# Kernel tuning notes

Measured on AMD Instinct MI355X. Metric: run time of the kernel, lower is better.

## Reference

```python
import jax, jax.numpy as jnp
import numpy as np
import math

P, DD, N, E, NDRUGS = 256, 128, 1024, 250000, 200000
BASELINE = 6.0

def _prelu(x, a):
    return jnp.where(x >= 0, x, a * x)

def _lrelu(x):
    return jnp.where(x >= 0, x, 0.2 * x)

def _lin(x, W, b):
    return x @ W.T + b

def setup_inputs() -> dict:
    key = jax.random.key(0)
    ks = jax.random.split(key, 40)
    f32 = jnp.float32
    inp = {}
    inp["target_features"] = jax.random.normal(ks[0], (P,), f32)
    inp["form_features"] = jax.random.normal(ks[1], (N, P), f32)
    inp["role_features"] = jax.random.normal(ks[2], (N, P), f32)
    inp["form_neighbors"] = jnp.arange(N, dtype=jnp.int32)
    inp["form_binds_src"] = jax.random.randint(ks[3], (E,), 0, N, jnp.int32)
    inp["form_binds_dst"] = jax.random.randint(ks[4], (E,), 0, NDRUGS, jnp.int32)
    inp["form_binds_y"] = jax.random.uniform(ks[5], (E,), f32, 4.0, 9.0)
    inp["role_neighbors"] = jnp.arange(N, dtype=jnp.int32)
    inp["role_binds_src"] = jax.random.randint(ks[6], (E,), 0, N, jnp.int32)
    inp["role_binds_dst"] = jax.random.randint(ks[7], (E,), 0, NDRUGS, jnp.int32)
    inp["role_binds_y"] = jax.random.uniform(ks[8], (E,), f32, 4.0, 9.0)
    inp["drug_features"] = jax.random.normal(ks[9], (NDRUGS, DD), f32)
    s = 0.02
    # prot_refiner: Linear(P,P) -> PReLU -> Linear(P,P)
    inp["Wr1"] = jax.random.normal(ks[10], (P, P), f32) * s
    inp["br1"] = jnp.zeros((P,), f32)
    inp["ar1"] = jnp.asarray(0.25, f32)
    inp["Wr2"] = jax.random.normal(ks[11], (P, P), f32) * s
    inp["br2"] = jnp.zeros((P,), f32)
    # q/k/v projections
    inp["Wq"] = jax.random.normal(ks[12], (DD, P), f32) * s
    inp["bq"] = jnp.zeros((DD,), f32)
    inp["Wk"] = jax.random.normal(ks[13], (DD, DD), f32) * s
    inp["bk"] = jnp.zeros((DD,), f32)
    inp["Wv"] = jax.random.normal(ks[14], (DD, DD), f32) * s
    inp["bv"] = jnp.zeros((DD,), f32)
    inp["layer_emb"] = jax.random.normal(ks[15], (2, 16), f32) * s
    # attn_net: (2P+16)->128->64->1 with LeakyReLU(0.2)
    inp["Wa1"] = jax.random.normal(ks[16], (128, 2 * P + 16), f32) * s
    inp["ba1"] = jnp.zeros((128,), f32)
    inp["Wa2"] = jax.random.normal(ks[17], (64, 128), f32) * s
    inp["ba2"] = jnp.zeros((64,), f32)
    inp["Wa3"] = jax.random.normal(ks[18], (1, 64), f32) * s
    inp["ba3"] = jnp.zeros((1,), f32)
    # integration_mlp: Linear(DD,P) -> PReLU -> Linear(P,P)
    inp["Wi1"] = jax.random.normal(ks[19], (P, DD), f32) * s
    inp["bi1"] = jnp.zeros((P,), f32)
    inp["ai"] = jnp.asarray(0.25, f32)
    inp["Wi2"] = jax.random.normal(ks[20], (P, P), f32) * s
    inp["bi2"] = jnp.zeros((P,), f32)
    inp["ln_g"] = jnp.ones((P,), f32)
    inp["ln_b"] = jnp.zeros((P,), f32)
    return inp

def reference(target_features, form_features, role_features, form_neighbors,
              form_binds_src, form_binds_dst, form_binds_y,
              role_neighbors, role_binds_src, role_binds_dst, role_binds_y,
              drug_features,
              Wr1, br1, ar1, Wr2, br2, Wq, bq, Wk, bk, Wv, bv, layer_emb,
              Wa1, ba1, Wa2, ba2, Wa3, ba3, Wi1, bi1, ai, Wi2, bi2, ln_g, ln_b):
    def refine(x):
        return _lin(_prelu(_lin(x, Wr1, br1), ar1), Wr2, br2)

    zt = refine(target_features)          # [P]
    zf = refine(form_features)            # [N, P]
    zr = refine(role_features)            # [N, P]
    Qv = _lin(zt, Wq, bq)                 # [DD]

    def build_msgs(neighbors, src, dst, y):
        # segment id for each edge: position of src in (sorted) neighbor_ids;
        # edges whose src is not a neighbor go to the dummy segment n.
        n = neighbors.shape[0]
        pos = jnp.clip(jnp.searchsorted(neighbors, src), 0, n - 1)
        seg = jnp.where(neighbors[pos] == src, pos, n)
        d = drug_features[dst]                                # [E, DD] gather
        K = _lin(d, Wk, bk)                                   # [E, DD]
        V = _lin(d, Wv, bv) * (y - BASELINE)[:, None]         # [E, DD]
        s = (K @ Qv) / math.sqrt(DD)                          # [E]
        nseg = n + 1
        m = jax.ops.segment_max(s, seg, num_segments=nseg)    # per-neighbor max
        ex = jnp.exp(s - m[seg])                              # stable softmax numerator
        den = jax.ops.segment_sum(ex, seg, num_segments=nseg)[:n]          # [N]
        num = jax.ops.segment_sum(ex[:, None] * V, seg, num_segments=nseg)[:n]  # [N, DD]
        return jnp.where(den[:, None] > 0, num / jnp.maximum(den, 1e-30)[:, None], 0.0)

    form_msgs = build_msgs(form_neighbors, form_binds_src, form_binds_dst, form_binds_y)
    role_msgs = build_msgs(role_neighbors, role_binds_src, role_binds_dst, role_binds_y)

    def attn(zn, layer_id):
        n = zn.shape[0]
        le = jnp.broadcast_to(layer_emb[layer_id], (n, 16))
        zt_e = jnp.broadcast_to(zt, (n, P))
        x = jnp.concatenate([zt_e, zn, le], axis=-1)          # [N, 2P+16]
        h = _lrelu(_lin(x, Wa1, ba1))
        h = _lrelu(_lin(h, Wa2, ba2))
        return _lin(h, Wa3, ba3)                              # [N, 1]

    all_msgs = jnp.concatenate([form_msgs, role_msgs], axis=0)   # [2N, DD]
    all_attn = jnp.concatenate([attn(zf, 0), attn(zr, 1)], axis=0)  # [2N, 1]
    w = jax.nn.softmax(all_attn, axis=0)
    v_prior = jnp.sum(w * all_msgs, axis=0)                   # [DD]
    integ = _lin(_prelu(_lin(v_prior, Wi1, bi1), ai), Wi2, bi2)
    x = zt + integ
    mu = jnp.mean(x, axis=-1, keepdims=True)
    var = jnp.var(x, axis=-1, keepdims=True)
    z = (x - mu) / jnp.sqrt(var + 1e-5) * ln_g + ln_b
    return (z, form_msgs, role_msgs)
```

## Files before the change

kernel.cpp:

```cpp
#include <hip/hip_runtime.h>

#define NP 256
#define NDD 128
#define NN 1024
#define NE 250000
#define SB 62

__global__ __launch_bounds__(256) void refine_kernel(
    const float* __restrict__ tgt, const float* __restrict__ formf, const float* __restrict__ rolef,
    const float* __restrict__ Wr1, const float* __restrict__ br1, const float* __restrict__ ar1,
    const float* __restrict__ Wr2, const float* __restrict__ br2,
    float* __restrict__ zt, float* __restrict__ zf, float* __restrict__ zr)
{
  __shared__ float X[4][NP];
  __shared__ float H[4][NP];
  const int t = threadIdx.x;
  const int base = blockIdx.x * 4;
  #pragma unroll
  for (int r = 0; r < 4; r++){
    int row = base + r;
    if (row < 2*NN + 1){
      const float* xp;
      if (row == 0)        xp = tgt;
      else if (row <= NN)  xp = formf + (size_t)(row-1)*NP;
      else                 xp = rolef + (size_t)(row-NN-1)*NP;
      X[r][t] = xp[t];
    } else {
      X[r][t] = 0.f;
    }
  }
  __syncthreads();
  const float a1 = ar1[0];
  float acc[4];
  #pragma unroll
  for (int r = 0; r < 4; r++) acc[r] = 0.f;
  const float4* w1p = reinterpret_cast<const float4*>(Wr1) + t*(NP/4);
  for (int k4 = 0; k4 < NP/4; k4++){
    float4 w = w1p[k4];
    #pragma unroll
    for (int r = 0; r < 4; r++){
      float4 xv = *reinterpret_cast<const float4*>(&X[r][k4*4]);
      acc[r] = fmaf(w.x, xv.x, acc[r]);
      acc[r] = fmaf(w.y, xv.y, acc[r]);
      acc[r] = fmaf(w.z, xv.z, acc[r]);
      acc[r] = fmaf(w.w, xv.w, acc[r]);
    }
  }
  const float b1 = br1[t];
  #pragma unroll
  for (int r = 0; r < 4; r++){
    float h = acc[r] + b1;
    H[r][t] = h >= 0.f ? h : a1*h;
  }
  __syncthreads();
  #pragma unroll
  for (int r = 0; r < 4; r++) acc[r] = 0.f;
  const float4* w2p = reinterpret_cast<const float4*>(Wr2) + t*(NP/4);
  for (int k4 = 0; k4 < NP/4; k4++){
    float4 w = w2p[k4];
    #pragma unroll
    for (int r = 0; r < 4; r++){
      float4 hv = *reinterpret_cast<const float4*>(&H[r][k4*4]);
      acc[r] = fmaf(w.x, hv.x, acc[r]);
      acc[r] = fmaf(w.y, hv.y, acc[r]);
      acc[r] = fmaf(w.z, hv.z, acc[r]);
      acc[r] = fmaf(w.w, hv.w, acc[r]);
    }
  }
  const float b2 = br2[t];
  #pragma unroll
  for (int r = 0; r < 4; r++){
    int row = base + r;
    if (row < 2*NN + 1){
      float v = acc[r] + b2;
      float* op;
      if (row == 0)        op = zt;
      else if (row <= NN)  op = zf + (size_t)(row-1)*NP;
      else                 op = zr + (size_t)(row-NN-1)*NP;
      op[t] = v;
    }
  }
}

__global__ __launch_bounds__(128) void qk_kernel(
    const float* __restrict__ zt,
    const float* __restrict__ Wq, const float* __restrict__ bq,
    const float* __restrict__ Wk, const float* __restrict__ bk,
    float* __restrict__ qk, float* __restrict__ s0)
{
  __shared__ float Z[NP];
  __shared__ float Q[NDD];
  __shared__ float red[NDD];
  int t = threadIdx.x;
  Z[t] = zt[t]; Z[t+128] = zt[t+128];
  __syncthreads();
  float acc = 0.f;
  const float4* wq = reinterpret_cast<const float4*>(Wq) + t*(NP/4);
  for (int k4 = 0; k4 < NP/4; k4++){
    float4 w = wq[k4];
    float4 zv = *reinterpret_cast<const float4*>(&Z[k4*4]);
    acc = fmaf(w.x, zv.x, fmaf(w.y, zv.y, fmaf(w.z, zv.z, fmaf(w.w, zv.w, acc))));
  }
  float qv = acc + bq[t];
  Q[t] = qv;
  __syncthreads();
  float a2 = 0.f;
  for (int j = 0; j < NDD; j++) a2 = fmaf(Wk[j*NDD + t], Q[j], a2);
  const float rs = 0.08838834764831845f;
  qk[t] = a2 * rs;
  red[t] = bk[t] * qv;
  __syncthreads();
  for (int o = 64; o; o >>= 1){ if (t < o) red[t] += red[t+o]; __syncthreads(); }
  if (t == 0) s0[0] = red[0] * rs;
}

__device__ __forceinline__ int seg_of(const int* NB, int s){
  if ((unsigned)s < NN && NB[s] == s) return s;
  int lo = 0, hi = NN;
  while (lo < hi){ int mid = (lo+hi)>>1; if (NB[mid] < s) lo = mid+1; else hi = mid; }
  return lo < NN ? lo : NN-1;
}

__global__ __launch_bounds__(1024) void hist_kernel(
    const int* __restrict__ neighF, const int* __restrict__ srcF,
    const int* __restrict__ neighR, const int* __restrict__ srcR,
    int* __restrict__ count)
{
  __shared__ int NB[NN];
  __shared__ int lh[NN];
  int bi = blockIdx.x;
  int role = bi >= SB ? 1 : 0;
  int blk = bi - role*SB;
  const int* neigh = role ? neighR : neighF;
  const int* src   = role ? srcR   : srcF;
  int* cnt = count + role*NN;
  int t = threadIdx.x;
  NB[t] = neigh[t];
  lh[t] = 0;
  __syncthreads();
  #pragma unroll
  for (int i = 0; i < 4; i++){
    int e = blk*4096 + i*1024 + t;
    if (e < NE){
      int s = src[e];
      int pos = seg_of(NB, s);
      if (NB[pos] == s) atomicAdd(&lh[pos], 1);
    }
  }
  __syncthreads();
  int c = lh[t];
  if (c > 0) atomicAdd(&cnt[t], c);
}

__global__ __launch_bounds__(1024) void scan_kernel(
    const int* __restrict__ count, int* __restrict__ offsets, int* __restrict__ cursor)
{
  __shared__ int s[NN];
  int l = blockIdx.x;
  int t = threadIdx.x;
  int c = count[l*NN + t];
  s[t] = c; __syncthreads();
  for (int o = 1; o < NN; o <<= 1){
    int v = (t >= o) ? s[t-o] : 0;
    __syncthreads();
    s[t] += v;
    __syncthreads();
  }
  int ex = s[t] - c;
  offsets[l*NN + t] = ex;
  cursor[l*NN + t]  = ex;
}

__global__ __launch_bounds__(1024) void scatter_kernel(
    const int* __restrict__ neighF, const int* __restrict__ srcF,
    const int* __restrict__ dstF, const float* __restrict__ yF,
    const int* __restrict__ neighR, const int* __restrict__ srcR,
    const int* __restrict__ dstR, const float* __restrict__ yR,
    int* __restrict__ cursor, int2* __restrict__ edges)
{
  __shared__ int NB[NN];
  __shared__ int lcur[NN];
  __shared__ int lbase[NN];
  int bi = blockIdx.x;
  int role = bi >= SB ? 1 : 0;
  int blk = bi - role*SB;
  const int* neigh = role ? neighR : neighF;
  const int* src   = role ? srcR   : srcF;
  const int* dst   = role ? dstR   : dstF;
  const float* yb  = role ? yR     : yF;
  int* cur  = cursor + role*NN;
  int2* ed  = edges  + (size_t)role*NE;
  int t = threadIdx.x;
  NB[t] = neigh[t];
  lcur[t] = 0;
  __syncthreads();
  int segr[4], locr[4]; int2 edr[4];
  #pragma unroll
  for (int i = 0; i < 4; i++){
    int e = blk*4096 + i*1024 + t;
    segr[i] = -1;
    if (e < NE){
      int s = src[e];
      int pos = seg_of(NB, s);
      if (NB[pos] == s){
        segr[i] = pos;
        edr[i]  = make_int2(dst[e], __float_as_int(yb[e]));
        locr[i] = atomicAdd(&lcur[pos], 1);
      }
    }
  }
  __syncthreads();
  int c = lcur[t];
  if (c > 0) lbase[t] = atomicAdd(&cur[t], c);
  __syncthreads();
  #pragma unroll
  for (int i = 0; i < 4; i++){
    if (segr[i] >= 0){
      ed[(size_t)(lbase[segr[i]] + locr[i])] = edr[i];
    }
  }
}

__global__ __launch_bounds__(256) void seg_kernel(
    const float* __restrict__ drug,
    const int2* __restrict__ edges,
    const int* __restrict__ offsets, const int* __restrict__ count,
    const float* __restrict__ qk, const float* __restrict__ s0p,
    float* __restrict__ g, float* __restrict__ den, float* __restrict__ cfac)
{
  int b = blockIdx.x;
  int tid = threadIdx.x;
  int w = tid >> 6, lane = tid & 63, l32 = lane & 31, half = lane >> 5;
  int off = offsets[b], cnt = count[b];
  int l = b >> 10;
  const int2* eb = edges + (size_t)l*NE;
  float4 q = reinterpret_cast<const float4*>(qk)[l32];
  float s0 = s0p[0];
  int chunk = (cnt + 3) >> 2;
  int start = w*chunk;
  int end = min(start + chunk, cnt);
  float dn = 0.f, cc = 0.f;
  float4 ga = make_float4(0.f,0.f,0.f,0.f);
  for (int i = start; i < end; i += 8){
    int dstp[4]; float yp[4]; bool vp[4];
    #pragma unroll
    for (int p2 = 0; p2 < 4; p2++){
      int idx = i + 2*p2 + half;
      bool v = idx < end;
      int2 e = eb[off + (v ? idx : start)];
      dstp[p2] = e.x; yp[p2] = __int_as_float(e.y); vp[p2] = v;
    }
    float4 dv[4];
    #pragma unroll
    for (int p2 = 0; p2 < 4; p2++){
      dv[p2] = reinterpret_cast<const float4*>(drug + (size_t)dstp[p2]*NDD)[l32];
    }
    #pragma unroll
    for (int p2 = 0; p2 < 4; p2++){
      float4 d = dv[p2];
      float s = fmaf(d.x, q.x, fmaf(d.y, q.y, fmaf(d.z, q.z, d.w*q.w)));
      s += __shfl_xor(s, 16, 64);
      s += __shfl_xor(s,  8, 64);
      s += __shfl_xor(s,  4, 64);
      s += __shfl_xor(s,  2, 64);
      s += __shfl_xor(s,  1, 64);
      float ex = vp[p2] ? __expf(s + s0) : 0.f;
      float wv = ex * (yp[p2] - 6.0f);
      dn += ex; cc += wv;
      ga.x = fmaf(wv, d.x, ga.x);
      ga.y = fmaf(wv, d.y, ga.y);
      ga.z = fmaf(wv, d.z, ga.z);
      ga.w = fmaf(wv, d.w, ga.w);
    }
  }
  __shared__ float4 sG[8][32];
  __shared__ float sD[8], sC[8];
  int slot = w*2 + half;
  sG[slot][l32] = ga;
  if (l32 == 0){ sD[slot] = dn; sC[slot] = cc; }
  __syncthreads();
  if (tid < NDD){
    int a = tid >> 2, c = tid & 3;
    float v = 0.f;
    #pragma unroll
    for (int k = 0; k < 8; k++)
      v += reinterpret_cast<const float*>(&sG[k][a])[c];
    g[(size_t)b*NDD + tid] = v;
    if (tid == 0){
      float ds = 0.f, cs = 0.f;
      #pragma unroll
      for (int k = 0; k < 8; k++){ ds += sD[k]; cs += sC[k]; }
      den[b] = ds; cfac[b] = cs;
    }
  }
}

__global__ __launch_bounds__(128) void msgs_kernel(
    const float* __restrict__ g, const float* __restrict__ den, const float* __restrict__ cfac,
    const float* __restrict__ Wv, const float* __restrict__ bv,
    float* __restrict__ msgsf, float* __restrict__ outm)
{
  __shared__ float G[8][NDD];
  int t = threadIdx.x;
  int base = blockIdx.x*8;
  #pragma unroll
  for (int r = 0; r < 8; r++) G[r][t] = g[(size_t)(base+r)*NDD + t];
  __syncthreads();
  float acc[8];
  #pragma unroll
  for (int r = 0; r < 8; r++) acc[r] = 0.f;
  const float4* wv4 = reinterpret_cast<const float4*>(Wv) + t*(NDD/4);
  for (int k4 = 0; k4 < NDD/4; k4++){
    float4 w = wv4[k4];
    #pragma unroll
    for (int r = 0; r < 8; r++){
      float4 gv = *reinterpret_cast<const float4*>(&G[r][k4*4]);
      acc[r] = fmaf(w.x, gv.x, acc[r]);
      acc[r] = fmaf(w.y, gv.y, acc[r]);
      acc[r] = fmaf(w.z, gv.z, acc[r]);
      acc[r] = fmaf(w.w, gv.w, acc[r]);
    }
  }
  float bvj = bv[t];
  #pragma unroll
  for (int r = 0; r < 8; r++){
    int row = base + r;
    float dn = den[row];
    float v = 0.f;
    if (dn > 0.f) v = (acc[r] + bvj*cfac[row]) / fmaxf(dn, 1e-30f);
    msgsf[(size_t)row*NDD + t] = v;
    outm [(size_t)row*NDD + t] = v;
  }
}

__global__ __launch_bounds__(256) void attn_kernel(
    const float* __restrict__ zt, const float* __restrict__ zf, const float* __restrict__ zr,
    const float* __restrict__ lemb,
    const float* __restrict__ Wa1, const float* __restrict__ ba1,
    const float* __restrict__ Wa2, const float* __restrict__ ba2,
    const float* __restrict__ Wa3, const float* __restrict__ ba3,
    float* __restrict__ attn)
{
  __shared__ float X[8][528];
  __shared__ float H1[8][NDD];
  int t = threadIdx.x;
  int tt = t & 127, grp = t >> 7;
  int base = blockIdx.x*8;
  for (int r = 0; r < 8; r++){
    int i = base + r;
    int layer = i >> 10, nn = i & (NN-1);
    const float* zn = (layer == 0) ? (zf + (size_t)nn*NP) : (zr + (size_t)nn*NP);
    for (int idx = t; idx < 528; idx += 256){
      float v;
      if (idx < NP)        v = zt[idx];
      else if (idx < 2*NP) v = zn[idx - NP];
      else                 v = lemb[layer*16 + (idx - 2*NP)];
      X[r][idx] = v;
    }
  }
  __syncthreads();
  float acc[4];
  #pragma unroll
  for (int r = 0; r < 4; r++) acc[r] = 0.f;
  const float4* w1 = reinterpret_cast<const float4*>(Wa1) + tt*(528/4);
  for (int k4 = 0; k4 < 132; k4++){
    float4 w = w1[k4];
    #pragma unroll
    for (int r = 0; r < 4; r++){
      float4 xv = *reinterpret_cast<const float4*>(&X[grp*4 + r][k4*4]);
      acc[r] = fmaf(w.x, xv.x, acc[r]);
      acc[r] = fmaf(w.y, xv.y, acc[r]);
      acc[r] = fmaf(w.z, xv.z, acc[r]);
      acc[r] = fmaf(w.w, xv.w, acc[r]);
    }
  }
  float b1 = ba1[tt];
  #pragma unroll
  for (int r = 0; r < 4; r++){
    float h = acc[r] + b1;
    H1[grp*4 + r][tt] = h >= 0.f ? h : 0.2f*h;
  }
  __syncthreads();
  if (tt < 64){
    float acc2[4];
    #pragma unroll
    for (int r = 0; r < 4; r++) acc2[r] = 0.f;
    const float4* w2 = reinterpret_cast<const float4*>(Wa2) + tt*(NDD/4);
    for (int k4 = 0; k4 < NDD/4; k4++){
      float4 w = w2[k4];
      #pragma unroll
      for (int r = 0; r < 4; r++){
        float4 hv = *reinterpret_cast<const float4*>(&H1[grp*4 + r][k4*4]);
        acc2[r] = fmaf(w.x, hv.x, acc2[r]);
        acc2[r] = fmaf(w.y, hv.y, acc2[r]);
        acc2[r] = fmaf(w.z, hv.z, acc2[r]);
        acc2[r] = fmaf(w.w, hv.w, acc2[r]);
      }
    }
    float b2 = ba2[tt];
    float w3 = Wa3[tt];
    float b3 = ba3[0];
    #pragma unroll
    for (int r = 0; r < 4; r++){
      float h = acc2[r] + b2;
      h = h >= 0.f ? h : 0.2f*h;
      float p = w3 * h;
      #pragma unroll
      for (int o = 32; o; o >>= 1) p += __shfl_xor(p, o, 64);
      if (tt == 0) attn[base + grp*4 + r] = p + b3;
    }
  }
}

__global__ __launch_bounds__(1024) void vprior_kernel(
    const float* __restrict__ attn, const float* __restrict__ msgsf, float* __restrict__ vp)
{
  __shared__ float A[2*NN];
  __shared__ float red[1024];
  __shared__ float Pp[8][NDD];
  int t = threadIdx.x;
  A[t] = attn[t]; A[t+1024] = attn[t+1024];
  __syncthreads();
  float mx = fmaxf(A[t], A[t+1024]);
  red[t] = mx; __syncthreads();
  for (int o = 512; o; o >>= 1){ if (t < o) red[t] = fmaxf(red[t], red[t+o]); __syncthreads(); }
  float M = red[0]; __syncthreads();
  float sm = __expf(A[t] - M) + __expf(A[t+1024] - M);
  red[t] = sm; __syncthreads();
  for (int o = 512; o; o >>= 1){ if (t < o) red[t] += red[t+o]; __syncthreads(); }
  float inv = 1.f / red[0]; __syncthreads();
  A[t]      = __expf(A[t]      - M) * inv;
  A[t+1024] = __expf(A[t+1024] - M) * inv;
  __syncthreads();
  int j = t & 127, grp = t >> 7;
  float acc = 0.f;
  int i0 = grp * 256;
  for (int i = i0; i < i0 + 256; i++) acc = fmaf(A[i], msgsf[(size_t)i*NDD + j], acc);
  Pp[grp][j] = acc;
  __syncthreads();
  if (t < NDD){
    float v = 0.f;
    #pragma unroll
    for (int gg = 0; gg < 8; gg++) v += Pp[gg][t];
    vp[t] = v;
  }
}

__global__ __launch_bounds__(256) void final_kernel(
    const float* __restrict__ vprior, const float* __restrict__ zt,
    const float* __restrict__ Wi1, const float* __restrict__ bi1, const float* __restrict__ ai,
    const float* __restrict__ Wi2, const float* __restrict__ bi2,
    const float* __restrict__ ln_g, const float* __restrict__ ln_b,
    float* __restrict__ zout)
{
  __shared__ float V[NDD];
  __shared__ float T1[NP];
  __shared__ float red[NP];
  int t = threadIdx.x;
  if (t < NDD) V[t] = vprior[t];
  __syncthreads();
  float acc = 0.f;
  const float4* w1 = reinterpret_cast<const float4*>(Wi1) + t*(NDD/4);
  for (int k4 = 0; k4 < NDD/4; k4++){
    float4 w = w1[k4];
    float4 vv = *reinterpret_cast<const float4*>(&V[k4*4]);
    acc = fmaf(w.x, vv.x, fmaf(w.y, vv.y, fmaf(w.z, vv.z, fmaf(w.w, vv.w, acc))));
  }
  float h = acc + bi1[t];
  float a = ai[0];
  T1[t] = h >= 0.f ? h : a*h;
  __syncthreads();
  float acc2 = 0.f;
  const float4* w2 = reinterpret_cast<const float4*>(Wi2) + t*(NP/4);
  for (int k4 = 0; k4 < NP/4; k4++){
    float4 w = w2[k4];
    float4 hv = *reinterpret_cast<const float4*>(&T1[k4*4]);
    acc2 = fmaf(w.x, hv.x, fmaf(w.y, hv.y, fmaf(w.z, hv.z, fmaf(w.w, hv.w, acc2))));
  }
  float x = zt[t] + acc2 + bi2[t];
  red[t] = x; __syncthreads();
  for (int o = 128; o; o >>= 1){ if (t < o) red[t] += red[t+o]; __syncthreads(); }
  float mu = red[0] * (1.f/256.f); __syncthreads();
  float d = x - mu;
  red[t] = d*d; __syncthreads();
  for (int o = 128; o; o >>= 1){ if (t < o) red[t] += red[t+o]; __syncthreads(); }
  float var = red[0] * (1.f/256.f);
  float zz = d * rsqrtf(var + 1e-5f) * ln_g[t] + ln_b[t];
  zout[t] = zz;
}

extern "C" void kernel_launch(void* const* d_in, const int* in_sizes, int n_in,
                              void* d_out, int out_size, void* d_ws, size_t ws_size,
                              hipStream_t stream)
{
  const float* tgt    = (const float*)d_in[0];
  const float* formf  = (const float*)d_in[1];
  const float* rolef  = (const float*)d_in[2];
  const int* fneigh   = (const int*)d_in[3];
  const int* fsrc     = (const int*)d_in[4];
  const int* fdst     = (const int*)d_in[5];
  const float* fy     = (const float*)d_in[6];
  const int* rneigh   = (const int*)d_in[7];
  const int* rsrc     = (const int*)d_in[8];
  const int* rdst     = (const int*)d_in[9];
  const float* ry     = (const float*)d_in[10];
  const float* drug   = (const float*)d_in[11];
  const float* Wr1 = (const float*)d_in[12];
  const float* br1 = (const float*)d_in[13];
  const float* ar1 = (const float*)d_in[14];
  const float* Wr2 = (const float*)d_in[15];
  const float* br2 = (const float*)d_in[16];
  const float* Wq  = (const float*)d_in[17];
  const float* bq  = (const float*)d_in[18];
  const float* Wk  = (const float*)d_in[19];
  const float* bk  = (const float*)d_in[20];
  const float* Wv  = (const float*)d_in[21];
  const float* bv  = (const float*)d_in[22];
  const float* lemb= (const float*)d_in[23];
  const float* Wa1 = (const float*)d_in[24];
  const float* ba1 = (const float*)d_in[25];
  const float* Wa2 = (const float*)d_in[26];
  const float* ba2 = (const float*)d_in[27];
  const float* Wa3 = (const float*)d_in[28];
  const float* ba3 = (const float*)d_in[29];
  const float* Wi1 = (const float*)d_in[30];
  const float* bi1 = (const float*)d_in[31];
  const float* ai  = (const float*)d_in[32];
  const float* Wi2 = (const float*)d_in[33];
  const float* bi2 = (const float*)d_in[34];
  const float* lng = (const float*)d_in[35];
  const float* lnb = (const float*)d_in[36];
  (void)in_sizes; (void)n_in; (void)out_size; (void)ws_size;

  float* ws = (float*)d_ws;
  float* zt_     = ws + 0;
  float* zf_     = ws + 256;
  float* zr_     = ws + 262400;
  float* qk_     = ws + 524544;
  float* s0_     = ws + 524672;
  float* attn_   = ws + 524800;
  float* vprior_ = ws + 526848;
  float* den_    = ws + 527104;
  float* cfac_   = ws + 529152;
  float* g_      = ws + 531200;
  float* msgsf_  = ws + 793344;
  int*   count_  = (int*)(ws + 1055488);
  int*   offs_   = (int*)(ws + 1057536);
  int*   cursor_ = (int*)(ws + 1059584);
  int2*  edges_  = (int2*)(ws + 1061632);

  hipMemsetAsync(count_, 0, 2*NN*sizeof(int), stream);

  refine_kernel<<<513, 256, 0, stream>>>(tgt, formf, rolef, Wr1, br1, ar1, Wr2, br2,
                                         zt_, zf_, zr_);
  qk_kernel<<<1, 128, 0, stream>>>(zt_, Wq, bq, Wk, bk, qk_, s0_);

  hist_kernel<<<2*SB, 1024, 0, stream>>>(fneigh, fsrc, rneigh, rsrc, count_);
  scan_kernel<<<2, 1024, 0, stream>>>(count_, offs_, cursor_);
  scatter_kernel<<<2*SB, 1024, 0, stream>>>(fneigh, fsrc, fdst, fy,
                                            rneigh, rsrc, rdst, ry,
                                            cursor_, edges_);

  seg_kernel<<<2*NN, 256, 0, stream>>>(drug, edges_, offs_, count_, qk_, s0_,
                                       g_, den_, cfac_);

  msgs_kernel<<<2*NN/8, 128, 0, stream>>>(g_, den_, cfac_, Wv, bv,
                                          msgsf_, (float*)d_out + NP);
  attn_kernel<<<2*NN/8, 256, 0, stream>>>(zt_, zf_, zr_, lemb,
                                          Wa1, ba1, Wa2, ba2, Wa3, ba3, attn_);
  vprior_kernel<<<1, 1024, 0, stream>>>(attn_, msgsf_, vprior_);
  final_kernel<<<1, 256, 0, stream>>>(vprior_, zt_, Wi1, bi1, ai, Wi2, bi2,
                                      lng, lnb, (float*)d_out);
}
```

Measured before the change: 389.2 us.

## Fuse small kernels to cut launch count: refine+qk, scan into scatter, attn+msgs

Merges qk into refine block 0 and moves the count/cursor zeroing into refine blocks 1 and 2, which replaces the memset. The prefix scan now runs redundantly in every scatter block, with a zeroed cursor added to the computed offsets. attn and msgs become one launch that splits its blocks by role, and vprior is fused with final. Together these remove four launches and one memset, at the cost of the scan being repeated in every scatter block and a single-block serial tail.

```diff
diff --git a/kernel.cpp b/kernel.cpp
--- a/kernel.cpp
+++ b/kernel.cpp
@@ -6,16 +6,32 @@
 #define NE 250000
 #define SB 62
 
-__global__ __launch_bounds__(256) void refine_kernel(
+__global__ __launch_bounds__(256) void refine_qk_kernel(
     const float* __restrict__ tgt, const float* __restrict__ formf, const float* __restrict__ rolef,
     const float* __restrict__ Wr1, const float* __restrict__ br1, const float* __restrict__ ar1,
     const float* __restrict__ Wr2, const float* __restrict__ br2,
-    float* __restrict__ zt, float* __restrict__ zf, float* __restrict__ zr)
+    const float* __restrict__ Wq, const float* __restrict__ bq,
+    const float* __restrict__ Wk, const float* __restrict__ bk,
+    float* __restrict__ zt, float* __restrict__ zf, float* __restrict__ zr,
+    float* __restrict__ qk, float* __restrict__ s0,
+    int* __restrict__ count, int* __restrict__ cursor0)
 {
   __shared__ float X[4][NP];
   __shared__ float H[4][NP];
+  __shared__ float Zs[NP];
+  __shared__ float Q[NDD];
+  __shared__ float red[NDD];
   const int t = threadIdx.x;
   const int base = blockIdx.x * 4;
+
+  if (blockIdx.x == 1){
+    #pragma unroll
+    for (int i = 0; i < 8; i++) count[t + i*256] = 0;
+  } else if (blockIdx.x == 2){
+    #pragma unroll
+    for (int i = 0; i < 8; i++) cursor0[t + i*256] = 0;
+  }
+
   #pragma unroll
   for (int r = 0; r < 4; r++){
     int row = base + r;
@@ -74,44 +90,40 @@
     if (row < 2*NN + 1){
       float v = acc[r] + b2;
       float* op;
-      if (row == 0)        op = zt;
+      if (row == 0){ op = zt; Zs[t] = v; }
       else if (row <= NN)  op = zf + (size_t)(row-1)*NP;
       else                 op = zr + (size_t)(row-NN-1)*NP;
       op[t] = v;
     }
   }
-}
-
-__global__ __launch_bounds__(128) void qk_kernel(
-    const float* __restrict__ zt,
-    const float* __restrict__ Wq, const float* __restrict__ bq,
-    const float* __restrict__ Wk, const float* __restrict__ bk,
-    float* __restrict__ qk, float* __restrict__ s0)
-{
-  __shared__ float Z[NP];
-  __shared__ float Q[NDD];
-  __shared__ float red[NDD];
-  int t = threadIdx.x;
-  Z[t] = zt[t]; Z[t+128] = zt[t+128];
-  __syncthreads();
-  float acc = 0.f;
-  const float4* wq = reinterpret_cast<const float4*>(Wq) + t*(NP/4);
-  for (int k4 = 0; k4 < NP/4; k4++){
-    float4 w = wq[k4];
-    float4 zv = *reinterpret_cast<const float4*>(&Z[k4*4]);
-    acc = fmaf(w.x, zv.x, fmaf(w.y, zv.y, fmaf(w.z, zv.z, fmaf(w.w, zv.w, acc))));
-  }
-  float qv = acc + bq[t];
-  Q[t] = qv;
-  __syncthreads();
-  float a2 = 0.f;
-  for (int j = 0; j < NDD; j++) a2 = fmaf(Wk[j*NDD + t], Q[j], a2);
-  const float rs = 0.08838834764831845f;
-  qk[t] = a2 * rs;
-  red[t] = bk[t] * qv;
-  __syncthreads();
-  for (int o = 64; o; o >>= 1){ if (t < o) red[t] += red[t+o]; __syncthreads(); }
-  if (t == 0) s0[0] = red[0] * rs;
+
+  if (blockIdx.x == 0){
+    __syncthreads();
+    if (t < NDD){
+      float a = 0.f;
+      const float4* wq = reinterpret_cast<const float4*>(Wq) + t*(NP/4);
+      for (int k4 = 0; k4 < NP/4; k4++){
+        float4 w = wq[k4];
+        float4 zv = *reinterpret_cast<const float4*>(&Zs[k4*4]);
+        a = fmaf(w.x, zv.x, fmaf(w.y, zv.y, fmaf(w.z, zv.z, fmaf(w.w, zv.w, a))));
+      }
+      float qv = a + bq[t];
+      Q[t] = qv;
+      red[t] = bk[t] * qv;
+    }
+    __syncthreads();
+    const float rs = 0.08838834764831845f;
+    if (t < NDD){
+      float a2 = 0.f;
+      for (int j = 0; j < NDD; j++) a2 = fmaf(Wk[j*NDD + t], Q[j], a2);
+      qk[t] = a2 * rs;
+    }
+    for (int o = 64; o; o >>= 1){
+      if (t < o) red[t] += red[t+o];
+      __syncthreads();
+    }
+    if (t == 0) s0[0] = red[0] * rs;
+  }
 }
 
 __device__ __forceinline__ int seg_of(const int* NB, int s){
@@ -152,34 +164,18 @@
   if (c > 0) atomicAdd(&cnt[t], c);
 }
 
-__global__ __launch_bounds__(1024) void scan_kernel(
-    const int* __restrict__ count, int* __restrict__ offsets, int* __restrict__ cursor)
-{
-  __shared__ int s[NN];
-  int l = blockIdx.x;
-  int t = threadIdx.x;
-  int c = count[l*NN + t];
-  s[t] = c; __syncthreads();
-  for (int o = 1; o < NN; o <<= 1){
-    int v = (t >= o) ? s[t-o] : 0;
-    __syncthreads();
-    s[t] += v;
-    __syncthreads();
-  }
-  int ex = s[t] - c;
-  offsets[l*NN + t] = ex;
-  cursor[l*NN + t]  = ex;
-}
-
 __global__ __launch_bounds__(1024) void scatter_kernel(
     const int* __restrict__ neighF, const int* __restrict__ srcF,
     const int* __restrict__ dstF, const float* __restrict__ yF,
     const int* __restrict__ neighR, const int* __restrict__ srcR,
     const int* __restrict__ dstR, const float* __restrict__ yR,
-    int* __restrict__ cursor, int2* __restrict__ edges)
+    const int* __restrict__ count, int* __restrict__ cursor0,
+    int* __restrict__ offsets, int2* __restrict__ edges)
 {
   __shared__ int NB[NN];
   __shared__ int lcur[NN];
+  __shared__ int sscan[NN];
+  __shared__ int obase[NN];
   __shared__ int lbase[NN];
   int bi = blockIdx.x;
   int role = bi >= SB ? 1 : 0;
@@ -188,12 +184,24 @@
   const int* src   = role ? srcR   : srcF;
   const int* dst   = role ? dstR   : dstF;
   const float* yb  = role ? yR     : yF;
-  int* cur  = cursor + role*NN;
-  int2* ed  = edges  + (size_t)role*NE;
+  int* cur0 = cursor0 + role*NN;
+  int2* ed  = edges   + (size_t)role*NE;
   int t = threadIdx.x;
   NB[t] = neigh[t];
   lcur[t] = 0;
-  __syncthreads();
+  int c0 = count[role*NN + t];
+  sscan[t] = c0;
+  __syncthreads();
+  for (int o = 1; o < NN; o <<= 1){
+    int v = (t >= o) ? sscan[t-o] : 0;
+    __syncthreads();
+    sscan[t] += v;
+    __syncthreads();
+  }
+  obase[t] = sscan[t] - c0;
+  if (blk == 0) offsets[role*NN + t] = sscan[t] - c0;
+  __syncthreads();
+
   int segr[4], locr[4]; int2 edr[4];
   #pragma unroll
   for (int i = 0; i < 4; i++){
@@ -211,7 +219,7 @@
   }
   __syncthreads();
   int c = lcur[t];
-  if (c > 0) lbase[t] = atomicAdd(&cur[t], c);
+  if (c > 0) lbase[t] = obase[t] + atomicAdd(&cur0[t], c);
   __syncthreads();
   #pragma unroll
   for (int i = 0; i < 4; i++){
@@ -295,129 +303,134 @@
   }
 }
 
-__global__ __launch_bounds__(128) void msgs_kernel(
-    const float* __restrict__ g, const float* __restrict__ den, const float* __restrict__ cfac,
-    const float* __restrict__ Wv, const float* __restrict__ bv,
-    float* __restrict__ msgsf, float* __restrict__ outm)
-{
-  __shared__ float G[8][NDD];
-  int t = threadIdx.x;
-  int base = blockIdx.x*8;
-  #pragma unroll
-  for (int r = 0; r < 8; r++) G[r][t] = g[(size_t)(base+r)*NDD + t];
-  __syncthreads();
-  float acc[8];
-  #pragma unroll
-  for (int r = 0; r < 8; r++) acc[r] = 0.f;
-  const float4* wv4 = reinterpret_cast<const float4*>(Wv) + t*(NDD/4);
-  for (int k4 = 0; k4 < NDD/4; k4++){
-    float4 w = wv4[k4];
-    #pragma unroll
-    for (int r = 0; r < 8; r++){
-      float4 gv = *reinterpret_cast<const float4*>(&G[r][k4*4]);
-      acc[r] = fmaf(w.x, gv.x, acc[r]);
-      acc[r] = fmaf(w.y, gv.y, acc[r]);
-      acc[r] = fmaf(w.z, gv.z, acc[r]);
-      acc[r] = fmaf(w.w, gv.w, acc[r]);
-    }
-  }
-  float bvj = bv[t];
-  #pragma unroll
-  for (int r = 0; r < 8; r++){
-    int row = base + r;
-    float dn = den[row];
-    float v = 0.f;
-    if (dn > 0.f) v = (acc[r] + bvj*cfac[row]) / fmaxf(dn, 1e-30f);
-    msgsf[(size_t)row*NDD + t] = v;
-    outm [(size_t)row*NDD + t] = v;
-  }
-}
-
-__global__ __launch_bounds__(256) void attn_kernel(
+__global__ __launch_bounds__(256) void attn_msgs_kernel(
     const float* __restrict__ zt, const float* __restrict__ zf, const float* __restrict__ zr,
     const float* __restrict__ lemb,
     const float* __restrict__ Wa1, const float* __restrict__ ba1,
     const float* __restrict__ Wa2, const float* __restrict__ ba2,
     const float* __restrict__ Wa3, const float* __restrict__ ba3,
-    float* __restrict__ attn)
-{
-  __shared__ float X[8][528];
-  __shared__ float H1[8][NDD];
+    const float* __restrict__ g, const float* __restrict__ den, const float* __restrict__ cfac,
+    const float* __restrict__ Wv, const float* __restrict__ bv,
+    float* __restrict__ attn, float* __restrict__ msgsf, float* __restrict__ outm)
+{
   int t = threadIdx.x;
   int tt = t & 127, grp = t >> 7;
-  int base = blockIdx.x*8;
-  for (int r = 0; r < 8; r++){
-    int i = base + r;
-    int layer = i >> 10, nn = i & (NN-1);
-    const float* zn = (layer == 0) ? (zf + (size_t)nn*NP) : (zr + (size_t)nn*NP);
-    for (int idx = t; idx < 528; idx += 256){
-      float v;
-      if (idx < NP)        v = zt[idx];
-      else if (idx < 2*NP) v = zn[idx - NP];
-      else                 v = lemb[layer*16 + (idx - 2*NP)];
-      X[r][idx] = v;
-    }
-  }
-  __syncthreads();
-  float acc[4];
-  #pragma unroll
-  for (int r = 0; r < 4; r++) acc[r] = 0.f;
-  const float4* w1 = reinterpret_cast<const float4*>(Wa1) + tt*(528/4);
-  for (int k4 = 0; k4 < 132; k4++){
-    float4 w = w1[k4];
-    #pragma unroll
-    for (int r = 0; r < 4; r++){
-      float4 xv = *reinterpret_cast<const float4*>(&X[grp*4 + r][k4*4]);
-      acc[r] = fmaf(w.x, xv.x, acc[r]);
-      acc[r] = fmaf(w.y, xv.y, acc[r]);
-      acc[r] = fmaf(w.z, xv.z, acc[r]);
-      acc[r] = fmaf(w.w, xv.w, acc[r]);
-    }
-  }
-  float b1 = ba1[tt];
-  #pragma unroll
-  for (int r = 0; r < 4; r++){
-    float h = acc[r] + b1;
-    H1[grp*4 + r][tt] = h >= 0.f ? h : 0.2f*h;
-  }
-  __syncthreads();
-  if (tt < 64){
-    float acc2[4];
-    #pragma unroll
-    for (int r = 0; r < 4; r++) acc2[r] = 0.f;
-    const float4* w2 = reinterpret_cast<const float4*>(Wa2) + tt*(NDD/4);
-    for (int k4 = 0; k4 < NDD/4; k4++){
-      float4 w = w2[k4];
+  if (blockIdx.x < 256){
+    __shared__ float X[8][528];
+    __shared__ float H1[8][NDD];
+    int base = blockIdx.x*8;
+    for (int r = 0; r < 8; r++){
+      int i = base + r;
+      int layer = i >> 10, nn = i & (NN-1);
+      const float* zn = (layer == 0) ? (zf + (size_t)nn*NP) : (zr + (size_t)nn*NP);
+      for (int idx = t; idx < 528; idx += 256){
+        float v;
+        if (idx < NP)        v = zt[idx];
+        else if (idx < 2*NP) v = zn[idx - NP];
+        else                 v = lemb[layer*16 + (idx - 2*NP)];
+        X[r][idx] = v;
+      }
+    }
+    __syncthreads();
+    float acc[4];
+    #pragma unroll
+    for (int r = 0; r < 4; r++) acc[r] = 0.f;
+    const float4* w1 = reinterpret_cast<const float4*>(Wa1) + tt*(528/4);
+    for (int k4 = 0; k4 < 132; k4++){
+      float4 w = w1[k4];
       #pragma unroll
       for (int r = 0; r < 4; r++){
-        float4 hv = *reinterpret_cast<const float4*>(&H1[grp*4 + r][k4*4]);
-        acc2[r] = fmaf(w.x, hv.x, acc2[r]);
-        acc2[r] = fmaf(w.y, hv.y, acc2[r]);
-        acc2[r] = fmaf(w.z, hv.z, acc2[r]);
-        acc2[r] = fmaf(w.w, hv.w, acc2[r]);
-      }
-    }
-    float b2 = ba2[tt];
-    float w3 = Wa3[tt];
-    float b3 = ba3[0];
+        float4 xv = *reinterpret_cast<const float4*>(&X[grp*4 + r][k4*4]);
+        acc[r] = fmaf(w.x, xv.x, acc[r]);
+        acc[r] = fmaf(w.y, xv.y, acc[r]);
+        acc[r] = fmaf(w.z, xv.z, acc[r]);
+        acc[r] = fmaf(w.w, xv.w, acc[r]);
+      }
+    }
+    float b1 = ba1[tt];
     #pragma unroll
     for (int r = 0; r < 4; r++){
-      float h = acc2[r] + b2;
-      h = h >= 0.f ? h : 0.2f*h;
-      float p = w3 * h;
+      float h = acc[r] + b1;
+      H1[grp*4 + r][tt] = h >= 0.f ? h : 0.2f*h;
+    }
+    __syncthreads();
+    if (tt < 64){
+      float acc2[4];
       #pragma unroll
-      for (int o = 32; o; o >>= 1) p += __shfl_xor(p, o, 64);
-      if (tt == 0) attn[base + grp*4 + r] = p + b3;
-    }
-  }
-}
-
-__global__ __launch_bounds__(1024) void vprior_kernel(
-    const float* __restrict__ attn, const float* __restrict__ msgsf, float* __restrict__ vp)
+      for (int r = 0; r < 4; r++) acc2[r] = 0.f;
+      const float4* w2 = reinterpret_cast<const float4*>(Wa2) + tt*(NDD/4);
+      for (int k4 = 0; k4 < NDD/4; k4++){
+        float4 w = w2[k4];
+        #pragma unroll
+        for (int r = 0; r < 4; r++){
+          float4 hv = *reinterpret_cast<const float4*>(&H1[grp*4 + r][k4*4]);
+          acc2[r] = fmaf(w.x, hv.x, acc2[r]);
+          acc2[r] = fmaf(w.y, hv.y, acc2[r]);
+          acc2[r] = fmaf(w.z, hv.z, acc2[r]);
+          acc2[r] = fmaf(w.w, hv.w, acc2[r]);
+        }
+      }
+      float b2 = ba2[tt];
+      float w3 = Wa3[tt];
+      float b3 = ba3[0];
+      #pragma unroll
+      for (int r = 0; r < 4; r++){
+        float h = acc2[r] + b2;
+        h = h >= 0.f ? h : 0.2f*h;
+        float p = w3 * h;
+        #pragma unroll
+        for (int o = 32; o; o >>= 1) p += __shfl_xor(p, o, 64);
+        if (tt == 0) attn[base + grp*4 + r] = p + b3;
+      }
+    }
+  } else {
+    __shared__ float G[8][NDD];
+    int base = (blockIdx.x - 256)*8;
+    #pragma unroll
+    for (int r = 0; r < 4; r++) G[grp*4 + r][tt] = g[(size_t)(base + grp*4 + r)*NDD + tt];
+    __syncthreads();
+    float acc[4];
+    #pragma unroll
+    for (int r = 0; r < 4; r++) acc[r] = 0.f;
+    const float4* wv4 = reinterpret_cast<const float4*>(Wv) + tt*(NDD/4);
+    for (int k4 = 0; k4 < NDD/4; k4++){
+      float4 w = wv4[k4];
+      #pragma unroll
+      for (int r = 0; r < 4; r++){
+        float4 gv = *reinterpret_cast<const float4*>(&G[grp*4 + r][k4*4]);
+        acc[r] = fmaf(w.x, gv.x, acc[r]);
+        acc[r] = fmaf(w.y, gv.y, acc[r]);
+        acc[r] = fmaf(w.z, gv.z, acc[r]);
+        acc[r] = fmaf(w.w, gv.w, acc[r]);
+      }
+    }
+    float bvj = bv[tt];
+    #pragma unroll
+    for (int r = 0; r < 4; r++){
+      int row = base + grp*4 + r;
+      float dn = den[row];
+      float v = 0.f;
+      if (dn > 0.f) v = (acc[r] + bvj*cfac[row]) / fmaxf(dn, 1e-30f);
+      msgsf[(size_t)row*NDD + tt] = v;
+      outm [(size_t)row*NDD + tt] = v;
+    }
+  }
+}
+
+__global__ __launch_bounds__(1024) void vprior_final_kernel(
+    const float* __restrict__ attn, const float* __restrict__ msgsf,
+    const float* __restrict__ zt,
+    const float* __restrict__ Wi1, const float* __restrict__ bi1, const float* __restrict__ ai,
+    const float* __restrict__ Wi2, const float* __restrict__ bi2,
+    const float* __restrict__ ln_g, const float* __restrict__ ln_b,
+    float* __restrict__ zout)
 {
   __shared__ float A[2*NN];
   __shared__ float red[1024];
   __shared__ float Pp[8][NDD];
+  __shared__ float V[NDD];
+  __shared__ float T1[NP];
+  __shared__ float red2[NP];
   int t = threadIdx.x;
   A[t] = attn[t]; A[t+1024] = attn[t+1024];
   __syncthreads();
@@ -442,51 +455,46 @@
     float v = 0.f;
     #pragma unroll
     for (int gg = 0; gg < 8; gg++) v += Pp[gg][t];
-    vp[t] = v;
-  }
-}
-
-__global__ __launch_bounds__(256) void final_kernel(
-    const float* __restrict__ vprior, const float* __restrict__ zt,
-    const float* __restrict__ Wi1, const float* __restrict__ bi1, const float* __restrict__ ai,
-    const float* __restrict__ Wi2, const float* __restrict__ bi2,
-    const float* __restrict__ ln_g, const float* __restrict__ ln_b,
-    float* __restrict__ zout)
-{
-  __shared__ float V[NDD];
-  __shared__ float T1[NP];
-  __shared__ float red[NP];
-  int t = threadIdx.x;
-  if (t < NDD) V[t] = vprior[t];
-  __syncthreads();
-  float acc = 0.f;
-  const float4* w1 = reinterpret_cast<const float4*>(Wi1) + t*(NDD/4);
-  for (int k4 = 0; k4 < NDD/4; k4++){
-    float4 w = w1[k4];
-    float4 vv = *reinterpret_cast<const float4*>(&V[k4*4]);
-    acc = fmaf(w.x, vv.x, fmaf(w.y, vv.y, fmaf(w.z, vv.z, fmaf(w.w, vv.w, acc))));
-  }
-  float h = acc + bi1[t];
-  float a = ai[0];
-  T1[t] = h >= 0.f ? h : a*h;
-  __syncthreads();
-  float acc2 = 0.f;
-  const float4* w2 = reinterpret_cast<const float4*>(Wi2) + t*(NP/4);
-  for (int k4 = 0; k4 < NP/4; k4++){
-    float4 w = w2[k4];
-    float4 hv = *reinterpret_cast<const float4*>(&T1[k4*4]);
-    acc2 = fmaf(w.x, hv.x, fmaf(w.y, hv.y, fmaf(w.z, hv.z, fmaf(w.w, hv.w, acc2))));
-  }
-  float x = zt[t] + acc2 + bi2[t];
-  red[t] = x; __syncthreads();
-  for (int o = 128; o; o >>= 1){ if (t < o) red[t] += red[t+o]; __syncthreads(); }
-  float mu = red[0] * (1.f/256.f); __syncthreads();
+    V[t] = v;
+  }
+  __syncthreads();
+  float x = 0.f;
+  if (t < NP){
+    float a1 = 0.f;
+    const float4* w1 = reinterpret_cast<const float4*>(Wi1) + t*(NDD/4);
+    for (int k4 = 0; k4 < NDD/4; k4++){
+      float4 w = w1[k4];
+      float4 vv = *reinterpret_cast<const float4*>(&V[k4*4]);
+      a1 = fmaf(w.x, vv.x, fmaf(w.y, vv.y, fmaf(w.z, vv.z, fmaf(w.w, vv.w, a1))));
+    }
+    float h = a1 + bi1[t];
+    float a = ai[0];
+    T1[t] = h >= 0.f ? h : a*h;
+  }
+  __syncthreads();
+  if (t < NP){
+    float a2 = 0.f;
+    const float4* w2 = reinterpret_cast<const float4*>(Wi2) + t*(NP/4);
+    for (int k4 = 0; k4 < NP/4; k4++){
+      float4 w = w2[k4];
+      float4 hv = *reinterpret_cast<const float4*>(&T1[k4*4]);
+      a2 = fmaf(w.x, hv.x, fmaf(w.y, hv.y, fmaf(w.z, hv.z, fmaf(w.w, hv.w, a2))));
+    }
+    x = zt[t] + a2 + bi2[t];
+    red2[t] = x;
+  }
+  __syncthreads();
+  for (int o = 128; o; o >>= 1){ if (t < o) red2[t] += red2[t+o]; __syncthreads(); }
+  float mu = red2[0] * (1.f/256.f); __syncthreads();
   float d = x - mu;
-  red[t] = d*d; __syncthreads();
-  for (int o = 128; o; o >>= 1){ if (t < o) red[t] += red[t+o]; __syncthreads(); }
-  float var = red[0] * (1.f/256.f);
-  float zz = d * rsqrtf(var + 1e-5f) * ln_g[t] + ln_b[t];
-  zout[t] = zz;
+  if (t < NP) red2[t] = d*d;
+  __syncthreads();
+  for (int o = 128; o; o >>= 1){ if (t < o) red2[t] += red2[t+o]; __syncthreads(); }
+  if (t < NP){
+    float var = red2[0] * (1.f/256.f);
+    float zz = d * rsqrtf(var + 1e-5f) * ln_g[t] + ln_b[t];
+    zout[t] = zz;
+  }
 }
 
 extern "C" void kernel_launch(void* const* d_in, const int* in_sizes, int n_in,
@@ -539,7 +547,6 @@
   float* qk_     = ws + 524544;
   float* s0_     = ws + 524672;
   float* attn_   = ws + 524800;
-  float* vprior_ = ws + 526848;
   float* den_    = ws + 527104;
   float* cfac_   = ws + 529152;
   float* g_      = ws + 531200;
@@ -549,26 +556,23 @@
   int*   cursor_ = (int*)(ws + 1059584);
   int2*  edges_  = (int2*)(ws + 1061632);
 
-  hipMemsetAsync(count_, 0, 2*NN*sizeof(int), stream);
-
-  refine_kernel<<<513, 256, 0, stream>>>(tgt, formf, rolef, Wr1, br1, ar1, Wr2, br2,
-                                         zt_, zf_, zr_);
-  qk_kernel<<<1, 128, 0, stream>>>(zt_, Wq, bq, Wk, bk, qk_, s0_);
+  refine_qk_kernel<<<513, 256, 0, stream>>>(tgt, formf, rolef, Wr1, br1, ar1, Wr2, br2,
+                                            Wq, bq, Wk, bk,
+                                            zt_, zf_, zr_, qk_, s0_, count_, cursor_);
 
   hist_kernel<<<2*SB, 1024, 0, stream>>>(fneigh, fsrc, rneigh, rsrc, count_);
-  scan_kernel<<<2, 1024, 0, stream>>>(count_, offs_, cursor_);
   scatter_kernel<<<2*SB, 1024, 0, stream>>>(fneigh, fsrc, fdst, fy,
                                             rneigh, rsrc, rdst, ry,
-                                            cursor_, edges_);
+                                            count_, cursor_, offs_, edges_);
 
   seg_kernel<<<2*NN, 256, 0, stream>>>(drug, edges_, offs_, count_, qk_, s0_,
                                        g_, den_, cfac_);
 
-  msgs_kernel<<<2*NN/8, 128, 0, stream>>>(g_, den_, cfac_, Wv, bv,
-                                          msgsf_, (float*)d_out + NP);
-  attn_kernel<<<2*NN/8, 256, 0, stream>>>(zt_, zf_, zr_, lemb,
-                                          Wa1, ba1, Wa2, ba2, Wa3, ba3, attn_);
-  vprior_kernel<<<1, 1024, 0, stream>>>(attn_, msgsf_, vprior_);
-  final_kernel<<<1, 256, 0, stream>>>(vprior_, zt_, Wi1, bi1, ai, Wi2, bi2,
-                                      lng, lnb, (float*)d_out);
-}
+  attn_msgs_kernel<<<512, 256, 0, stream>>>(zt_, zf_, zr_, lemb,
+                                            Wa1, ba1, Wa2, ba2, Wa3, ba3,
+                                            g_, den_, cfac_, Wv, bv,
+                                            attn_, msgsf_, (float*)d_out + NP);
+  vprior_final_kernel<<<1, 1024, 0, stream>>>(attn_, msgsf_, zt_,
+                                              Wi1, bi1, ai, Wi2, bi2,
+                                              lng, lnb, (float*)d_out);
+}
```

Measured after the change: 392.4 us. About the same (+0.8%).
